# Performance work log

Hardware: AMD Instinct MI355X
Metric: run time of the kernel (lower is better)

## Reference

```python
import jax, jax.numpy as jnp
import numpy as np

N = 100000
IN_DIM = 64
OUT_DIM = 64
NUM_TYPES = 64


def setup_inputs() -> dict:
    key = jax.random.key(0)
    kx, kt, km, kb = jax.random.split(key, 4)
    x = jax.random.normal(kx, (N, IN_DIM), dtype=jnp.float32)
    types = jax.random.randint(kt, (N,), 0, NUM_TYPES, dtype=jnp.int64)
    # kaiming_uniform with a=sqrt(5) -> bound = sqrt(6/((1+5)*fan_in)) = 1/sqrt(fan_in)
    w_bound = 1.0 / np.sqrt(IN_DIM)
    matrix = jax.random.uniform(km, (NUM_TYPES, IN_DIM, OUT_DIM), dtype=jnp.float32,
                                minval=-w_bound, maxval=w_bound)
    b_bound = 1.0 / np.sqrt(IN_DIM)
    bias = jax.random.uniform(kb, (NUM_TYPES, OUT_DIM), dtype=jnp.float32,
                              minval=-b_bound, maxval=b_bound)
    return {"x": x, "types": types, "matrix": matrix, "bias": bias}


def reference(x, types, matrix, bias):
    # Gather per-atom weight matrices: (N, in, out), then batched matvec.
    out = jnp.einsum('ni,nio->no', x, matrix[types])  # (N, out)
    out = out + bias[types]                            # per-type bias
    return out
```

## Files before the change

### kernel.cpp

```cpp
#include <hip/hip_runtime.h>
#include <hip/hip_bf16.h>

#define NTYPES 64
#define DIM 64
#define CAP 4096

typedef short bf16x8 __attribute__((ext_vector_type(8)));
typedef float f32x4  __attribute__((ext_vector_type(4)));

static __device__ __forceinline__ short f2bf(float f) {
    __hip_bfloat16 h = __float2bfloat16(f);
    return *reinterpret_cast<short*>(&h);
}

__global__ void scatter_mtr_k(const int* __restrict__ types, int n,
                              int* __restrict__ cursor, int* __restrict__ perm,
                              const float* __restrict__ M, short* __restrict__ Mt) {
    __shared__ int lh[NTYPES];
    __shared__ int lbase[NTYPES];
    int tid = threadIdx.x;
    int bid = blockIdx.x;
    if (tid < NTYPES) lh[tid] = 0;
    __syncthreads();

    const int PER = 4;
    int base = bid * blockDim.x * PER;
    int myt[PER], myo[PER];
    #pragma unroll
    for (int k = 0; k < PER; ++k) {
        int i = base + k * blockDim.x + tid;
        if (i < n) {
            myt[k] = types[i];
            myo[k] = atomicAdd(&lh[myt[k]], 1);
        } else myt[k] = -1;
    }
    __syncthreads();
    if (tid < NTYPES) lbase[tid] = lh[tid] ? atomicAdd(&cursor[tid], lh[tid]) : 0;
    __syncthreads();
    #pragma unroll
    for (int k = 0; k < PER; ++k)
        if (myt[k] >= 0)
            perm[myt[k] * CAP + lbase[myt[k]] + myo[k]] = base + k * blockDim.x + tid;

    if (bid < NTYPES) {
        int t  = bid;
        int o  = tid >> 2;
        int ks = tid & 3;
        const float* Ms = M + ((size_t)t << 12);
        short vals[16];
        #pragma unroll
        for (int j = 0; j < 16; ++j)
            vals[j] = f2bf(Ms[(ks * 16 + j) * DIM + o]);
        short* dst = Mt + ((size_t)t << 12) + o * DIM + ks * 16;
        *(bf16x8*)(dst)     = *(const bf16x8*)(vals);
        *(bf16x8*)(dst + 8) = *(const bf16x8*)(vals + 8);
    }
}

__global__ __launch_bounds__(256) void main_k(const float* __restrict__ x,
                                              const short* __restrict__ Mt,
                                              const float* __restrict__ bias,
                                              const int* __restrict__ cursor,
                                              const int* __restrict__ perm,
                                              float* __restrict__ out) {
    int t = blockIdx.x;
    int cnt = cursor[t];
    if (cnt <= 0) return;

    int tid  = threadIdx.x;
    int lane = tid & 63;
    int wv   = tid >> 6;
    int col  = lane & 15;
    int hi   = lane >> 4;

    const short* At = Mt + ((size_t)t << 12);
    bf16x8 a0[4], a1[4];
    f32x4  bsv[4];
    #pragma unroll
    for (int ct = 0; ct < 4; ++ct) {
        const short* ar = At + (ct * 16 + col) * DIM + hi * 8;
        a0[ct] = *(const bf16x8*)(ar);
        a1[ct] = *(const bf16x8*)(ar + 32);
        bsv[ct] = *(const f32x4*)(bias + t * DIM + ct * 16 + hi * 4);
    }

    const int* pbase = perm + t * CAP;
    int nt = (cnt + 15) >> 4;

    for (int tau = blockIdx.y * 4 + wv; tau < nt; tau += gridDim.y * 4) {
        int a = (tau << 4) + col;
        bool valid = a < cnt;
        if (!valid) a = cnt - 1;
        int g = pbase[a];

        const float* xr = x + ((size_t)g << 6);
        float4 p0 = *(const float4*)(xr + hi * 8);
        float4 p1 = *(const float4*)(xr + hi * 8 + 4);
        float4 p2 = *(const float4*)(xr + 32 + hi * 8);
        float4 p3 = *(const float4*)(xr + 32 + hi * 8 + 4);
        bf16x8 b0, b1;
        b0[0] = f2bf(p0.x); b0[1] = f2bf(p0.y); b0[2] = f2bf(p0.z); b0[3] = f2bf(p0.w);
        b0[4] = f2bf(p1.x); b0[5] = f2bf(p1.y); b0[6] = f2bf(p1.z); b0[7] = f2bf(p1.w);
        b1[0] = f2bf(p2.x); b1[1] = f2bf(p2.y); b1[2] = f2bf(p2.z); b1[3] = f2bf(p2.w);
        b1[4] = f2bf(p3.x); b1[5] = f2bf(p3.y); b1[6] = f2bf(p3.z); b1[7] = f2bf(p3.w);

        f32x4 acc[4];
        #pragma unroll
        for (int ct = 0; ct < 4; ++ct) {
            acc[ct] = bsv[ct];
            acc[ct] = __builtin_amdgcn_mfma_f32_16x16x32_bf16(a0[ct], b0, acc[ct], 0, 0, 0);
            acc[ct] = __builtin_amdgcn_mfma_f32_16x16x32_bf16(a1[ct], b1, acc[ct], 0, 0, 0);
        }

        if (valid) {
            float* orow = out + ((size_t)g << 6);
            #pragma unroll
            for (int ct = 0; ct < 4; ++ct)
                *(f32x4*)(orow + ct * 16 + hi * 4) = acc[ct];
        }
    }
}

extern "C" void kernel_launch(void* const* d_in, const int* in_sizes, int n_in,
                              void* d_out, int out_size, void* d_ws, size_t ws_size,
                              hipStream_t stream) {
    const float* x     = (const float*)d_in[0];
    const int*   types = (const int*)d_in[1];
    const float* M     = (const float*)d_in[2];
    const float* bias  = (const float*)d_in[3];
    float* out = (float*)d_out;
    int n = in_sizes[1];

    int* cursor = (int*)d_ws;
    int* perm   = cursor + 256;
    short* Mt   = (short*)(perm + NTYPES * CAP);

    hipMemsetAsync(cursor, 0, NTYPES * sizeof(int), stream);
    scatter_mtr_k<<<(n + 1023) / 1024, 256, 0, stream>>>(types, n, cursor, perm, M, Mt);
    main_k<<<dim3(NTYPES, 8), 256, 0, stream>>>(x, Mt, bias, cursor, perm, out);
}
```

Before: 95.49 us.

## Prefetch next x tile, vectorize type loads, widen grid, use nontemporal stores

The main kernel now loads the next gathered x tile before computing the current one, so memory latency overlaps with the MFMA work. Waves with no tile return before loading weights. The grid's y dimension doubles to 16, launch bounds request 4 blocks per CU, and output writes become nontemporal stores. The scatter kernel reads types as int4 with a contiguous per-thread layout. The cost is more registers held live for the prefetched tile.

```diff
diff --git a/kernel.cpp b/kernel.cpp
--- a/kernel.cpp
+++ b/kernel.cpp
@@ -24,15 +24,19 @@
     __syncthreads();
 
     const int PER = 4;
-    int base = bid * blockDim.x * PER;
+    int i0 = bid * blockDim.x * PER + tid * PER;
     int myt[PER], myo[PER];
-    #pragma unroll
-    for (int k = 0; k < PER; ++k) {
-        int i = base + k * blockDim.x + tid;
-        if (i < n) {
-            myt[k] = types[i];
-            myo[k] = atomicAdd(&lh[myt[k]], 1);
-        } else myt[k] = -1;
+    if (i0 + PER <= n) {
+        int4 tv = *(const int4*)(types + i0);
+        myt[0] = tv.x; myt[1] = tv.y; myt[2] = tv.z; myt[3] = tv.w;
+        #pragma unroll
+        for (int k = 0; k < PER; ++k) myo[k] = atomicAdd(&lh[myt[k]], 1);
+    } else {
+        #pragma unroll
+        for (int k = 0; k < PER; ++k) {
+            if (i0 + k < n) { myt[k] = types[i0 + k]; myo[k] = atomicAdd(&lh[myt[k]], 1); }
+            else myt[k] = -1;
+        }
     }
     __syncthreads();
     if (tid < NTYPES) lbase[tid] = lh[tid] ? atomicAdd(&cursor[tid], lh[tid]) : 0;
@@ -40,7 +44,7 @@
     #pragma unroll
     for (int k = 0; k < PER; ++k)
         if (myt[k] >= 0)
-            perm[myt[k] * CAP + lbase[myt[k]] + myo[k]] = base + k * blockDim.x + tid;
+            perm[myt[k] * CAP + lbase[myt[k]] + myo[k]] = i0 + k;
 
     if (bid < NTYPES) {
         int t  = bid;
@@ -57,12 +61,12 @@
     }
 }
 
-__global__ __launch_bounds__(256) void main_k(const float* __restrict__ x,
-                                              const short* __restrict__ Mt,
-                                              const float* __restrict__ bias,
-                                              const int* __restrict__ cursor,
-                                              const int* __restrict__ perm,
-                                              float* __restrict__ out) {
+__global__ __launch_bounds__(256, 4) void main_k(const float* __restrict__ x,
+                                                 const short* __restrict__ Mt,
+                                                 const float* __restrict__ bias,
+                                                 const int* __restrict__ cursor,
+                                                 const int* __restrict__ perm,
+                                                 float* __restrict__ out) {
     int t = blockIdx.x;
     int cnt = cursor[t];
     if (cnt <= 0) return;
@@ -72,6 +76,12 @@
     int wv   = tid >> 6;
     int col  = lane & 15;
     int hi   = lane >> 4;
+
+    const int* pbase = perm + t * CAP;
+    int nt = (cnt + 15) >> 4;
+    const int stride = gridDim.y * 4;
+    int tau = blockIdx.y * 4 + wv;
+    if (tau >= nt) return;
 
     const short* At = Mt + ((size_t)t << 12);
     bf16x8 a0[4], a1[4];
@@ -84,20 +94,33 @@
         bsv[ct] = *(const f32x4*)(bias + t * DIM + ct * 16 + hi * 4);
     }
 
-    const int* pbase = perm + t * CAP;
-    int nt = (cnt + 15) >> 4;
+    int a = (tau << 4) + col;
+    bool valid = a < cnt;
+    if (!valid) a = cnt - 1;
+    int g = pbase[a];
+    const float* xr = x + ((size_t)g << 6);
+    float4 p0 = *(const float4*)(xr + hi * 8);
+    float4 p1 = *(const float4*)(xr + hi * 8 + 4);
+    float4 p2 = *(const float4*)(xr + 32 + hi * 8);
+    float4 p3 = *(const float4*)(xr + 32 + hi * 8 + 4);
 
-    for (int tau = blockIdx.y * 4 + wv; tau < nt; tau += gridDim.y * 4) {
-        int a = (tau << 4) + col;
-        bool valid = a < cnt;
-        if (!valid) a = cnt - 1;
-        int g = pbase[a];
+    while (true) {
+        int tau_n = tau + stride;
+        bool have_n = tau_n < nt;
+        int g_n = 0; bool valid_n = false;
+        float4 q0, q1, q2, q3;
+        if (have_n) {
+            int an = (tau_n << 4) + col;
+            valid_n = an < cnt;
+            if (!valid_n) an = cnt - 1;
+            g_n = pbase[an];
+            const float* xrn = x + ((size_t)g_n << 6);
+            q0 = *(const float4*)(xrn + hi * 8);
+            q1 = *(const float4*)(xrn + hi * 8 + 4);
+            q2 = *(const float4*)(xrn + 32 + hi * 8);
+            q3 = *(const float4*)(xrn + 32 + hi * 8 + 4);
+        }
 
-        const float* xr = x + ((size_t)g << 6);
-        float4 p0 = *(const float4*)(xr + hi * 8);
-        float4 p1 = *(const float4*)(xr + hi * 8 + 4);
-        float4 p2 = *(const float4*)(xr + 32 + hi * 8);
-        float4 p3 = *(const float4*)(xr + 32 + hi * 8 + 4);
         bf16x8 b0, b1;
         b0[0] = f2bf(p0.x); b0[1] = f2bf(p0.y); b0[2] = f2bf(p0.z); b0[3] = f2bf(p0.w);
         b0[4] = f2bf(p1.x); b0[5] = f2bf(p1.y); b0[6] = f2bf(p1.z); b0[7] = f2bf(p1.w);
@@ -116,8 +139,12 @@
             float* orow = out + ((size_t)g << 6);
             #pragma unroll
             for (int ct = 0; ct < 4; ++ct)
-                *(f32x4*)(orow + ct * 16 + hi * 4) = acc[ct];
+                __builtin_nontemporal_store(acc[ct], (f32x4*)(orow + ct * 16 + hi * 4));
         }
+
+        if (!have_n) break;
+        tau = tau_n; g = g_n; valid = valid_n;
+        p0 = q0; p1 = q1; p2 = q2; p3 = q3;
     }
 }
 
@@ -137,5 +164,5 @@
 
     hipMemsetAsync(cursor, 0, NTYPES * sizeof(int), stream);
     scatter_mtr_k<<<(n + 1023) / 1024, 256, 0, stream>>>(types, n, cursor, perm, M, Mt);
-    main_k<<<dim3(NTYPES, 8), 256, 0, stream>>>(x, Mt, bias, cursor, perm, out);
+    main_k<<<dim3(NTYPES, 16), 256, 0, stream>>>(x, Mt, bias, cursor, perm, out);
 }
```

After: 94.22 us. Within noise of the previous version (-1.3%).
